# Kernel tuning notes

Measured on AMD Instinct MI355X. Metric: run time of the kernel, lower is better.

## Reference

```python
import jax, jax.numpy as jnp
import numpy as np
from jax import lax

HIDDEN = 16
DN = ('NCHW', 'OIHW', 'NCHW')

def setup_inputs() -> dict:
    key = jax.random.key(0)
    k1, k2, k3 = jax.random.split(key, 3)
    b, t, c, h, w = 8, 12, 5, 256, 256
    x = jax.random.normal(k1, (b, t, c, h, w), dtype=jnp.float32)
    # PyTorch-like init scale for conv weights
    W_cell = jax.random.normal(k2, (4 * HIDDEN, c + HIDDEN, 3, 3), dtype=jnp.float32) * 0.05
    b_cell = jnp.zeros((4 * HIDDEN,), dtype=jnp.float32)
    W_final = jax.random.normal(k3, (1, HIDDEN, 1, 1), dtype=jnp.float32) * 0.1
    b_final = jnp.zeros((1,), dtype=jnp.float32)
    return {"x": x, "W_cell": W_cell, "b_cell": b_cell,
            "W_final": W_final, "b_final": b_final}

def _cell_step(h_c, x_t, W_cell, b_cell):
    h_cur, c_cur = h_c
    combined = jnp.concatenate([x_t, h_cur], axis=1)          # [B, C+H, H, W]
    conv = lax.conv_general_dilated(combined, W_cell, (1, 1), 'SAME',
                                    dimension_numbers=DN)
    conv = conv + b_cell[None, :, None, None]                  # [B, 4H, H, W]
    cc_i, cc_f, cc_o, cc_g = jnp.split(conv, 4, axis=1)
    i = jax.nn.sigmoid(cc_i)
    f = jax.nn.sigmoid(cc_f)
    o = jax.nn.sigmoid(cc_o)
    g = jnp.tanh(cc_g)
    c_next = f * c_cur + i * g
    h_next = o * jnp.tanh(c_next)
    return h_next, c_next

def reference(x, W_cell, b_cell, W_final, b_final):
    b, t, c, hh, ww = x.shape
    h0 = jnp.zeros((b, HIDDEN, hh, ww), dtype=x.dtype)
    c0 = jnp.zeros((b, HIDDEN, hh, ww), dtype=x.dtype)
    xt = jnp.moveaxis(x, 1, 0)  # [T, B, C, H, W] for scan over time

    def step(carry, x_t):
        return _cell_step(carry, x_t, W_cell, b_cell), None

    (h_last, _), _ = lax.scan(step, (h0, c0), xt)
    out = lax.conv_general_dilated(h_last, W_final, (1, 1), 'SAME',
                                   dimension_numbers=DN)
    out = out + b_final[None, :, None, None]
    return out
```

## Files before the change

### kernel.cpp

```cpp
#include <hip/hip_runtime.h>
#include <math.h>

#define HIDDEN 16
#define CIN 5
#define BB 8
#define TT 12
#define HH 256
#define WW 256
#define TX 32
#define TY 8
#define HALO_X 34
#define HALO_Y 10
#define NPX (HALO_X * HALO_Y)
#define STRIDE 40
#define NBLK_PERSIST 1024
#define NTILES 2048

typedef __attribute__((ext_vector_type(8))) short bf16x8;
typedef __attribute__((ext_vector_type(4))) float floatx4;

__device__ __forceinline__ unsigned short f2bf(float f) {
    unsigned int u = __float_as_uint(f);
    u += 0x7fffu + ((u >> 16) & 1u);
    return (unsigned short)(u >> 16);
}
__device__ __forceinline__ float bf2f(unsigned short s) {
    return __uint_as_float(((unsigned int)s) << 16);
}
__device__ __forceinline__ float fast_sigmoid(float x) { return 1.0f / (1.0f + __expf(-x)); }
__device__ __forceinline__ float fast_tanh(float x) {
    float e2 = __expf(-2.0f * fabsf(x));
    float t = (1.0f - e2) / (1.0f + e2);
    return copysignf(t, x);
}

__global__ void prep_w_kernel(const float* __restrict__ Wc,
                              unsigned short* __restrict__ Wfrag) {
    int i = blockIdx.x * 256 + threadIdx.x;
    if (i >= 9 * 4 * 64 * 8) return;
    int j    = i & 7;
    int lane = (i >> 3) & 63;
    int g    = (i >> 9) & 3;
    int tap  = i >> 11;
    int k    = ((lane >> 4) << 3) + j;
    int col  = lane & 15;
    int o    = g * 16 + col;
    float w  = 0.0f;
    if (k < 21) {
        int ci_ref = (k < 16) ? (5 + k) : (k - 16);
        w = Wc[(o * 21 + ci_ref) * 9 + tap];
    }
    Wfrag[i] = f2bf(w);
}

__global__ void prep_x_kernel(const float* __restrict__ x,
                              unsigned short* __restrict__ xp) {
    size_t n = (size_t)blockIdx.x * 256 + threadIdx.x;
    const size_t TOTPX = (size_t)BB * TT * HH * WW;
    if (n >= TOTPX) return;
    size_t bt  = n / (size_t)(HH * WW);
    size_t pix = n - bt * (size_t)(HH * WW);
    const float* src = x + bt * (size_t)CIN * HH * WW + pix;
    unsigned short v[8];
    #pragma unroll
    for (int c = 0; c < CIN; ++c) v[c] = f2bf(src[(size_t)c * HH * WW]);
    v[5] = 0; v[6] = 0; v[7] = 0;
    *(uint4*)&xp[n * 8] = *(const uint4*)v;
}

__global__ void prep_flags_kernel(unsigned int* __restrict__ flags) {
    int i = blockIdx.x * 256 + threadIdx.x;
    if (i < NTILES) flags[i] = 0;
}

__global__ __launch_bounds__(256, 4)
void convlstm_persistent_kernel(const float* __restrict__ x,
                                const unsigned short* __restrict__ xp,
                                unsigned short* __restrict__ ha,
                                unsigned short* __restrict__ hbuf,
                                const unsigned short* __restrict__ Wfrag,
                                const float* __restrict__ bias,
                                const float* __restrict__ Wf,
                                const float* __restrict__ bfin,
                                float* __restrict__ out,
                                unsigned int* __restrict__ flags,
                                int use_xp) {
    __shared__ unsigned short tile[NPX * STRIDE];

    const int tid  = threadIdx.x;
    const int lane = tid & 63;
    const int wave = tid >> 6;
    const int u    = lane & 15;
    const int quad = lane >> 4;
    const int bid  = (int)blockIdx.x;

    int nb_id[2];
    unsigned nb_act = 0;
    {
        int s  = lane + (lane >= 4 ? 1 : 0);
        int dy = s / 3 - 1;
        int dx = s - (s / 3) * 3 - 1;
        #pragma unroll
        for (int tl = 0; tl < 2; ++tl) {
            int n  = bid + tl * NBLK_PERSIST;
            int tx = n & 7;
            int ty = (n >> 3) & 31;
            bool act = (lane < 8) && (tx + dx >= 0) && (tx + dx < 8)
                                  && (ty + dy >= 0) && (ty + dy < 32);
            nb_id[tl] = act ? (n + dy * 8 + dx) : 0;
            if (act) nb_act |= 1u << tl;
        }
    }

    int hof[2][2];
    int xof[2][2];
    int pixv[2][2];
    int bbv[2];
    unsigned inbm = 0;
    #pragma unroll
    for (int tl = 0; tl < 2; ++tl) {
        int n  = bid + tl * NBLK_PERSIST;
        int x0 = (n & 7) * TX;
        int y0 = ((n >> 3) & 31) * TY;
        int bb = n >> 8;
        bbv[tl] = bb;
        #pragma unroll
        for (int it = 0; it < 2; ++it) {
            int i  = tid + it * 256;
            int ly = i / HALO_X;
            int lx = i - ly * HALO_X;
            int gy = y0 + ly - 1;
            int gx = x0 + lx - 1;
            bool inb = (gy >= 0 && gy < HH && gx >= 0 && gx < WW) && (i < NPX);
            int pix = gy * WW + gx;
            pixv[tl][it] = pix;
            hof[tl][it]  = (bb * HH * WW + pix) * HIDDEN;
            xof[tl][it]  = (bb * TT * HH * WW + pix) * 8;
            if (inb) inbm |= 1u << (tl * 2 + it);
        }
    }

    float bg[4];
    #pragma unroll
    for (int g = 0; g < 4; ++g) bg[g] = bias[g * 16 + u];
    const float wfu = Wf[u];
    const float bf0 = bfin[0];

    float cA[2][2][4];
    float cB[2][2][4];
    #pragma unroll
    for (int a = 0; a < 2; ++a)
        #pragma unroll
        for (int m = 0; m < 2; ++m)
            #pragma unroll
            for (int r = 0; r < 4; ++r) { cA[a][m][r] = 0.0f; cB[a][m][r] = 0.0f; }

    #pragma unroll 1
    for (int t = 0; t < TT; ++t) {
        const unsigned short* h_in  = (t & 1) ? ha : hbuf;
        unsigned short*       h_out = (t & 1) ? hbuf : ha;
        const int first = (t == 0);
        const int last  = (t == TT - 1);

        #pragma unroll
        for (int tl = 0; tl < 2; ++tl) {
            const int n  = bid + tl * NBLK_PERSIST;
            const int x0 = (n & 7) * TX;
            const int y0 = ((n >> 3) & 31) * TY;
            const int bb = bbv[tl];

            if (t > 0) {
                if (wave == 0) {
                    const bool act = (nb_act >> tl) & 1;
                    const unsigned need = (unsigned)t;
                    for (;;) {
                        unsigned v = act
                            ? __hip_atomic_load(&flags[nb_id[tl]], __ATOMIC_RELAXED,
                                                __HIP_MEMORY_SCOPE_AGENT)
                            : 0xFFFFFFFFu;
                        if (__all(v >= need)) break;
                        __builtin_amdgcn_s_sleep(2);
                    }
                    if (tid == 0) __threadfence();
                }
                __syncthreads();
            } else if (tl == 1) {
                __syncthreads();
            }

            #pragma unroll
            for (int it = 0; it < 2; ++it) {
                if (it == 1 && tid >= NPX - 256) break;
                unsigned short* row = &tile[(tid + it * 256) * STRIDE];
                const bool inb = (inbm >> (tl * 2 + it)) & 1;
                uint4 z = {0, 0, 0, 0};
                if (inb && !first) {
                    const unsigned short* hp = h_in + hof[tl][it];
                    *(uint4*)&row[0] = *(const uint4*)&hp[0];
                    *(uint4*)&row[8] = *(const uint4*)&hp[8];
                } else {
                    *(uint4*)&row[0] = z;
                    *(uint4*)&row[8] = z;
                }
                if (use_xp) {
                    if (inb)
                        *(uint4*)&row[16] =
                            *(const uint4*)&xp[xof[tl][it] + t * (HH * WW * 8)];
                    else
                        *(uint4*)&row[16] = z;
                } else {
                    #pragma unroll
                    for (int ci = 0; ci < CIN; ++ci) {
                        float v = 0.0f;
                        if (inb) v = x[(((size_t)bb * TT + t) * CIN + ci) * (size_t)(HH * WW)
                                       + pixv[tl][it]];
                        row[16 + ci] = f2bf(v);
                    }
                    row[21] = 0; row[22] = 0; row[23] = 0;
                }
                *(uint4*)&row[24] = z;
            }
            __syncthreads();

            #pragma unroll 1
            for (int half = 0; half < 2; ++half) {
                floatx4 acc[2][4];
                int abase[2];
                #pragma unroll
                for (int mh = 0; mh < 2; ++mh) {
                    int ml = half * 2 + mh;
                    int m  = wave + ml * 4;
                    int my = m >> 1;
                    int mx = (m & 1) << 4;
                    abase[mh] = (my * HALO_X + mx + u) * STRIDE + quad * 8;
                    #pragma unroll
                    for (int g = 0; g < 4; ++g)
                        acc[mh][g] = (floatx4){bg[g], bg[g], bg[g], bg[g]};
                }

                #pragma unroll 3
                for (int tap = 0; tap < 9; ++tap) {
                    int ky = tap / 3;
                    int kx = tap - ky * 3;
                    int toff = (ky * HALO_X + kx) * STRIDE;
                    bf16x8 bfr[4];
                    #pragma unroll
                    for (int g = 0; g < 4; ++g)
                        bfr[g] = *(const bf16x8*)&Wfrag[(size_t)((tap * 4 + g) * 64 + lane) * 8];
                    #pragma unroll
                    for (int mh = 0; mh < 2; ++mh) {
                        bf16x8 af = *(const bf16x8*)&tile[abase[mh] + toff];
                        #pragma unroll
                        for (int g = 0; g < 4; ++g)
                            acc[mh][g] = __builtin_amdgcn_mfma_f32_16x16x32_bf16(
                                af, bfr[g], acc[mh][g], 0, 0, 0);
                    }
                }

                #pragma unroll
                for (int mh = 0; mh < 2; ++mh) {
                    int ml = half * 2 + mh;
                    int m  = wave + ml * 4;
                    int my = m >> 1;
                    int mx = (m & 1) << 4;
                    int py = y0 + my;
                    #pragma unroll
                    for (int r = 0; r < 4; ++r) {
                        int pxx = x0 + mx + quad * 4 + r;
                        float ig = fast_sigmoid(acc[mh][0][r]);
                        float fg = fast_sigmoid(acc[mh][1][r]);
                        float og = fast_sigmoid(acc[mh][2][r]);
                        float gg = fast_tanh(acc[mh][3][r]);
                        float c_old = half ? cB[tl][mh][r] : cA[tl][mh][r];
                        float c_new = fg * c_old + ig * gg;
                        if (half) cB[tl][mh][r] = c_new; else cA[tl][mh][r] = c_new;
                        float hval = og * fast_tanh(c_new);
                        if (last) {
                            float s = wfu * hval;
                            s += __shfl_xor(s, 1);
                            s += __shfl_xor(s, 2);
                            s += __shfl_xor(s, 4);
                            s += __shfl_xor(s, 8);
                            if (u == 0)
                                out[(size_t)bb * HH * WW + (size_t)py * WW + pxx] = s + bf0;
                        } else {
                            size_t idx = ((size_t)bb * HH * WW + (size_t)py * WW + pxx)
                                         * HIDDEN + u;
                            h_out[idx] = f2bf(hval);
                        }
                    }
                }
            }

            if (!last) {
                __syncthreads();
                if (tid == 0) {
                    __threadfence();
                    __hip_atomic_store(&flags[n], (unsigned)(t + 1), __ATOMIC_RELAXED,
                                       __HIP_MEMORY_SCOPE_AGENT);
                }
            }
        }
    }
}

__global__ __launch_bounds__(256, 5)
void convlstm_step_kernel(const float* __restrict__ x, int t,
                          const unsigned short* __restrict__ xp,
                          const unsigned short* __restrict__ h_in,
                          unsigned short* __restrict__ h_out,
                          float* __restrict__ c_state,
                          const unsigned short* __restrict__ Wfrag,
                          const float* __restrict__ bias,
                          int first, int use_xp) {
    __shared__ unsigned short tile[NPX * STRIDE];

    const int tid  = threadIdx.x;
    const int lane = tid & 63;
    const int wave = tid >> 6;
    const int x0 = blockIdx.x * TX;
    const int y0 = blockIdx.y * TY;
    const int bb = blockIdx.z;

    for (int i = tid; i < NPX; i += 256) {
        int ly = i / HALO_X;
        int lx = i - ly * HALO_X;
        int gy = y0 + ly - 1;
        int gx = x0 + lx - 1;
        bool inb = (gy >= 0 && gy < HH && gx >= 0 && gx < WW);
        unsigned short* row = &tile[i * STRIDE];
        uint4 z = {0, 0, 0, 0};
        if (inb && !first) {
            size_t hbase = ((size_t)bb * HH * WW + (size_t)gy * WW + gx) * HIDDEN;
            *(uint4*)&row[0] = *(const uint4*)&h_in[hbase];
            *(uint4*)&row[8] = *(const uint4*)&h_in[hbase + 8];
        } else {
            *(uint4*)&row[0] = z;
            *(uint4*)&row[8] = z;
        }
        if (use_xp) {
            if (inb) {
                size_t xb = (((size_t)bb * TT + t) * (size_t)(HH * WW)
                             + (size_t)gy * WW + gx) * 8;
                *(uint4*)&row[16] = *(const uint4*)&xp[xb];
            } else {
                *(uint4*)&row[16] = z;
            }
        } else {
            #pragma unroll
            for (int ci = 0; ci < CIN; ++ci) {
                float v = 0.0f;
                if (inb) v = x[(((size_t)bb * TT + t) * CIN + ci) * (size_t)(HH * WW)
                               + (size_t)gy * WW + gx];
                row[16 + ci] = f2bf(v);
            }
            row[21] = 0; row[22] = 0; row[23] = 0;
        }
        *(uint4*)&row[24] = z;
    }
    __syncthreads();

    const int u    = lane & 15;
    const int quad = lane >> 4;

    float bg[4];
    #pragma unroll
    for (int g = 0; g < 4; ++g) bg[g] = bias[g * 16 + u];

    #pragma unroll 1
    for (int half = 0; half < 2; ++half) {
        floatx4 acc[2][4];
        int abase[2];
        #pragma unroll
        for (int mh = 0; mh < 2; ++mh) {
            int ml = half * 2 + mh;
            int m  = wave + ml * 4;
            int my = m >> 1;
            int mx = (m & 1) << 4;
            abase[mh] = (my * HALO_X + mx + u) * STRIDE + quad * 8;
            #pragma unroll
            for (int g = 0; g < 4; ++g)
                acc[mh][g] = (floatx4){bg[g], bg[g], bg[g], bg[g]};
        }

        #pragma unroll 3
        for (int tap = 0; tap < 9; ++tap) {
            int ky = tap / 3;
            int kx = tap - ky * 3;
            int toff = (ky * HALO_X + kx) * STRIDE;
            bf16x8 bfr[4];
            #pragma unroll
            for (int g = 0; g < 4; ++g)
                bfr[g] = *(const bf16x8*)&Wfrag[(size_t)((tap * 4 + g) * 64 + lane) * 8];
            #pragma unroll
            for (int mh = 0; mh < 2; ++mh) {
                bf16x8 af = *(const bf16x8*)&tile[abase[mh] + toff];
                #pragma unroll
                for (int g = 0; g < 4; ++g)
                    acc[mh][g] = __builtin_amdgcn_mfma_f32_16x16x32_bf16(
                        af, bfr[g], acc[mh][g], 0, 0, 0);
            }
        }

        #pragma unroll
        for (int mh = 0; mh < 2; ++mh) {
            int ml = half * 2 + mh;
            int m  = wave + ml * 4;
            int my = m >> 1;
            int mx = (m & 1) << 4;
            int py = y0 + my;
            #pragma unroll
            for (int r = 0; r < 4; ++r) {
                int pxx = x0 + mx + quad * 4 + r;
                size_t idx = ((size_t)bb * HH * WW + (size_t)py * WW + pxx) * HIDDEN + u;
                float ig = fast_sigmoid(acc[mh][0][r]);
                float fg = fast_sigmoid(acc[mh][1][r]);
                float og = fast_sigmoid(acc[mh][2][r]);
                float gg = fast_tanh(acc[mh][3][r]);
                float c_old = first ? 0.0f : c_state[idx];
                float c_new = fg * c_old + ig * gg;
                c_state[idx] = c_new;
                h_out[idx] = f2bf(og * fast_tanh(c_new));
            }
        }
    }
}

__global__ void final_conv_kernel(const unsigned short* __restrict__ h,
                                  const float* __restrict__ Wf,
                                  const float* __restrict__ bf_,
                                  float* __restrict__ out) {
    int i = blockIdx.x * 256 + threadIdx.x;
    if (i >= BB * HH * WW) return;
    size_t base = (size_t)i * HIDDEN;
    uint4 v0 = *(const uint4*)&h[base];
    uint4 v1 = *(const uint4*)&h[base + 8];
    const unsigned short* p0 = (const unsigned short*)&v0;
    const unsigned short* p1 = (const unsigned short*)&v1;
    float s = bf_[0];
    #pragma unroll
    for (int k = 0; k < 8; ++k) s += Wf[k] * bf2f(p0[k]);
    #pragma unroll
    for (int k = 0; k < 8; ++k) s += Wf[8 + k] * bf2f(p1[k]);
    out[i] = s;
}

extern "C" void kernel_launch(void* const* d_in, const int* in_sizes, int n_in,
                              void* d_out, int out_size, void* d_ws, size_t ws_size,
                              hipStream_t stream) {
    const float* x  = (const float*)d_in[0];
    const float* Wc = (const float*)d_in[1];
    const float* bc = (const float*)d_in[2];
    const float* Wf = (const float*)d_in[3];
    const float* bf = (const float*)d_in[4];
    float* out = (float*)d_out;

    char* ws = (char*)d_ws;
    const size_t h_bytes = (size_t)BB * HH * WW * HIDDEN * 2;
    const size_t c_bytes = (size_t)BB * HH * WW * HIDDEN * 4;
    const size_t w_bytes = 9 * 4 * 64 * 8 * 2;
    const size_t f_bytes = (size_t)NTILES * 4;
    const size_t x_bytes = (size_t)BB * TT * HH * WW * 8 * 2;

    unsigned short* h_a = (unsigned short*)(ws);
    unsigned short* h_b = (unsigned short*)(ws + h_bytes);
    float* c            = (float*)(ws + 2 * h_bytes);
    unsigned short* Wfr = (unsigned short*)(ws + 2 * h_bytes + c_bytes);
    unsigned int* flags = (unsigned int*)(ws + 2 * h_bytes + c_bytes + w_bytes);
    unsigned short* xp  = (unsigned short*)(ws + 2 * h_bytes + c_bytes + w_bytes + f_bytes);

    const int use_xp =
        (ws_size >= 2 * h_bytes + c_bytes + w_bytes + f_bytes + x_bytes) ? 1 : 0;

    prep_w_kernel<<<(9 * 4 * 64 * 8 + 255) / 256, 256, 0, stream>>>(Wc, Wfr);
    prep_flags_kernel<<<(NTILES + 255) / 256, 256, 0, stream>>>(flags);
    if (use_xp) {
        size_t totpx = (size_t)BB * TT * HH * WW;
        prep_x_kernel<<<(int)((totpx + 255) / 256), 256, 0, stream>>>(x, xp);
    }

    int occ = 0;
    hipOccupancyMaxActiveBlocksPerMultiprocessor(&occ, convlstm_persistent_kernel,
                                                 256, 0);
    bool done = false;
    if (occ >= 4) {
        const unsigned short* xp_arg = use_xp ? xp : (const unsigned short*)0;
        int use_xp_arg = use_xp;
        void* kargs[] = {
            (void*)&x, (void*)&xp_arg, (void*)&h_a, (void*)&h_b,
            (void*)&Wfr, (void*)&bc, (void*)&Wf, (void*)&bf,
            (void*)&out, (void*)&flags, (void*)&use_xp_arg
        };
        if (hipLaunchCooperativeKernel((const void*)convlstm_persistent_kernel,
                                       dim3(NBLK_PERSIST, 1, 1), dim3(256, 1, 1),
                                       kargs, 0, stream) == hipSuccess)
            done = true;
    }

    if (!done) {
        dim3 grid(WW / TX, HH / TY, BB);
        dim3 block(256, 1, 1);
        const unsigned short* h_in = h_a;
        for (int t = 0; t < TT; ++t) {
            unsigned short* h_out = (t & 1) ? h_b : h_a;
            convlstm_step_kernel<<<grid, block, 0, stream>>>(
                x, t, use_xp ? xp : (const unsigned short*)0,
                h_in, h_out, c, Wfr, bc, (t == 0) ? 1 : 0, use_xp);
            h_in = h_out;
        }
        final_conv_kernel<<<(BB * HH * WW + 255) / 256, 256, 0, stream>>>(
            h_in, Wf, bf, out);
    }
}
```

Baseline: 700.4 us.

## Keep hidden state resident in LDS per tile, exchange only halo ring globally

New measurement: 688.7 us. Within noise of the previous version (-1.7%).

```diff
diff --git a/kernel.cpp b/kernel.cpp
--- a/kernel.cpp
+++ b/kernel.cpp
@@ -15,6 +15,9 @@
 #define STRIDE 40
 #define NBLK_PERSIST 1024
 #define NTILES 2048
+#define NRING 84
+#define ROWSH 24
+#define XSTEP (HH * WW * 8)
 
 typedef __attribute__((ext_vector_type(8))) short bf16x8;
 typedef __attribute__((ext_vector_type(4))) float floatx4;
@@ -27,8 +30,21 @@
 __device__ __forceinline__ float bf2f(unsigned short s) {
     return __uint_as_float(((unsigned int)s) << 16);
 }
-__device__ __forceinline__ float fast_sigmoid(float x) { return 1.0f / (1.0f + __expf(-x)); }
+__device__ __forceinline__ float rcpf(float x) {
+    float r;
+    asm("v_rcp_f32 %0, %1" : "=v"(r) : "v"(x));
+    return r;
+}
+__device__ __forceinline__ float fast_sigmoid(float x) {
+    return rcpf(1.0f + __expf(-x));
+}
 __device__ __forceinline__ float fast_tanh(float x) {
+    float e2 = __expf(-2.0f * fabsf(x));
+    float t = (1.0f - e2) * rcpf(1.0f + e2);
+    return copysignf(t, x);
+}
+__device__ __forceinline__ float leg_sigmoid(float x) { return 1.0f / (1.0f + __expf(-x)); }
+__device__ __forceinline__ float leg_tanh(float x) {
     float e2 = __expf(-2.0f * fabsf(x));
     float t = (1.0f - e2) / (1.0f + e2);
     return copysignf(t, x);
@@ -85,7 +101,8 @@
                                 float* __restrict__ out,
                                 unsigned int* __restrict__ flags,
                                 int use_xp) {
-    __shared__ unsigned short tile[NPX * STRIDE];
+    __shared__ unsigned short hx[2 * NPX * ROWSH + 8];
+    const int ZOFF = 2 * NPX * ROWSH;
 
     const int tid  = threadIdx.x;
     const int lane = tid & 63;
@@ -94,6 +111,16 @@
     const int quad = lane >> 4;
     const int bid  = (int)blockIdx.x;
 
+    int ntile[2], x0v[2], y0v[2], bbv[2];
+    #pragma unroll
+    for (int tl = 0; tl < 2; ++tl) {
+        int n = (bid & 7) * 256 + (bid >> 3) + tl * 128;
+        ntile[tl] = n;
+        x0v[tl] = (n & 7) * TX;
+        y0v[tl] = ((n >> 3) & 31) * TY;
+        bbv[tl] = n >> 8;
+    }
+
     int nb_id[2];
     unsigned nb_act = 0;
     {
@@ -102,7 +129,7 @@
         int dx = s - (s / 3) * 3 - 1;
         #pragma unroll
         for (int tl = 0; tl < 2; ++tl) {
-            int n  = bid + tl * NBLK_PERSIST;
+            int n  = ntile[tl];
             int tx = n & 7;
             int ty = (n >> 3) & 31;
             bool act = (lane < 8) && (tx + dx >= 0) && (tx + dx < 8)
@@ -112,39 +139,64 @@
         }
     }
 
-    int hof[2][2];
     int xof[2][2];
     int pixv[2][2];
-    int bbv[2];
     unsigned inbm = 0;
     #pragma unroll
     for (int tl = 0; tl < 2; ++tl) {
-        int n  = bid + tl * NBLK_PERSIST;
-        int x0 = (n & 7) * TX;
-        int y0 = ((n >> 3) & 31) * TY;
-        int bb = n >> 8;
-        bbv[tl] = bb;
         #pragma unroll
         for (int it = 0; it < 2; ++it) {
             int i  = tid + it * 256;
             int ly = i / HALO_X;
             int lx = i - ly * HALO_X;
-            int gy = y0 + ly - 1;
-            int gx = x0 + lx - 1;
+            int gy = y0v[tl] + ly - 1;
+            int gx = x0v[tl] + lx - 1;
             bool inb = (gy >= 0 && gy < HH && gx >= 0 && gx < WW) && (i < NPX);
             int pix = gy * WW + gx;
             pixv[tl][it] = pix;
-            hof[tl][it]  = (bb * HH * WW + pix) * HIDDEN;
-            xof[tl][it]  = (bb * TT * HH * WW + pix) * 8;
+            xof[tl][it]  = (bbv[tl] * TT * HH * WW + pix) * 8;
             if (inb) inbm |= 1u << (tl * 2 + it);
         }
     }
+
+    int rrow = 0;
+    int rgoff[2] = {0, 0};
+    unsigned ringm = 0;
+    if (tid < NRING) {
+        int ly, lx;
+        if (tid < 34)      { ly = 0;                lx = tid; }
+        else if (tid < 68) { ly = HALO_Y - 1;       lx = tid - 34; }
+        else { int k = tid - 68; ly = 1 + (k >> 1); lx = (k & 1) * (HALO_X - 1); }
+        rrow = ly * HALO_X + lx;
+        #pragma unroll
+        for (int tl = 0; tl < 2; ++tl) {
+            int gy = y0v[tl] + ly - 1;
+            int gx = x0v[tl] + lx - 1;
+            bool inb = (gy >= 0 && gy < HH && gx >= 0 && gx < WW);
+            rgoff[tl] = (bbv[tl] * HH * WW + gy * WW + gx) * HIDDEN;
+            if (inb) ringm |= 1u << tl;
+        }
+    }
+
+    uint4 xr0 = {0, 0, 0, 0}, xr1 = {0, 0, 0, 0};
+    if (use_xp) {
+        if (inbm & 1u) xr0 = *(const uint4*)&xp[xof[0][0]];
+        if (tid < NPX - 256 && (inbm & 2u)) xr1 = *(const uint4*)&xp[xof[0][1]];
+    }
+
+    for (int i = tid; i < 2 * NPX; i += 256) {
+        uint4 z = {0, 0, 0, 0};
+        *(uint4*)&hx[i * ROWSH]     = z;
+        *(uint4*)&hx[i * ROWSH + 8] = z;
+    }
+    if (tid == 0) { uint4 z = {0, 0, 0, 0}; *(uint4*)&hx[ZOFF] = z; }
 
     float bg[4];
     #pragma unroll
     for (int g = 0; g < 4; ++g) bg[g] = bias[g * 16 + u];
     const float wfu = Wf[u];
     const float bf0 = bfin[0];
+    const int msel  = (quad < 3) ? ROWSH : 0;
 
     float cA[2][2][4];
     float cB[2][2][4];
@@ -164,10 +216,11 @@
 
         #pragma unroll
         for (int tl = 0; tl < 2; ++tl) {
-            const int n  = bid + tl * NBLK_PERSIST;
-            const int x0 = (n & 7) * TX;
-            const int y0 = ((n >> 3) & 31) * TY;
-            const int bb = bbv[tl];
+            const int n   = ntile[tl];
+            const int x0  = x0v[tl];
+            const int y0  = y0v[tl];
+            const int bb  = bbv[tl];
+            const int TLB = tl * NPX * ROWSH;
 
             if (t > 0) {
                 if (wave == 0) {
@@ -184,55 +237,60 @@
                     if (tid == 0) __threadfence();
                 }
                 __syncthreads();
-            } else if (tl == 1) {
-                __syncthreads();
-            }
-
-            #pragma unroll
-            for (int it = 0; it < 2; ++it) {
-                if (it == 1 && tid >= NPX - 256) break;
-                unsigned short* row = &tile[(tid + it * 256) * STRIDE];
-                const bool inb = (inbm >> (tl * 2 + it)) & 1;
-                uint4 z = {0, 0, 0, 0};
-                if (inb && !first) {
-                    const unsigned short* hp = h_in + hof[tl][it];
-                    *(uint4*)&row[0] = *(const uint4*)&hp[0];
-                    *(uint4*)&row[8] = *(const uint4*)&hp[8];
-                } else {
-                    *(uint4*)&row[0] = z;
-                    *(uint4*)&row[8] = z;
-                }
-                if (use_xp) {
-                    if (inb)
-                        *(uint4*)&row[16] =
-                            *(const uint4*)&xp[xof[tl][it] + t * (HH * WW * 8)];
-                    else
-                        *(uint4*)&row[16] = z;
-                } else {
+            }
+
+            if (use_xp) {
+                *(uint4*)&hx[TLB + tid * ROWSH + 16] = xr0;
+                if (tid < NPX - 256)
+                    *(uint4*)&hx[TLB + (tid + 256) * ROWSH + 16] = xr1;
+            } else {
+                #pragma unroll
+                for (int it = 0; it < 2; ++it) {
+                    if (it == 1 && tid >= NPX - 256) break;
+                    const bool inb = (inbm >> (tl * 2 + it)) & 1;
+                    unsigned short v[8];
                     #pragma unroll
                     for (int ci = 0; ci < CIN; ++ci) {
-                        float v = 0.0f;
-                        if (inb) v = x[(((size_t)bb * TT + t) * CIN + ci) * (size_t)(HH * WW)
+                        float f = 0.0f;
+                        if (inb) f = x[(((size_t)bb * TT + t) * CIN + ci) * (size_t)(HH * WW)
                                        + pixv[tl][it]];
-                        row[16 + ci] = f2bf(v);
+                        v[ci] = f2bf(f);
                     }
-                    row[21] = 0; row[22] = 0; row[23] = 0;
-                }
-                *(uint4*)&row[24] = z;
+                    v[5] = 0; v[6] = 0; v[7] = 0;
+                    *(uint4*)&hx[TLB + (tid + it * 256) * ROWSH + 16] = *(const uint4*)v;
+                }
+            }
+            if (!first && tid < NRING && ((ringm >> tl) & 1)) {
+                const unsigned short* hp = h_in + rgoff[tl];
+                *(uint4*)&hx[TLB + rrow * ROWSH]     = *(const uint4*)&hp[0];
+                *(uint4*)&hx[TLB + rrow * ROWSH + 8] = *(const uint4*)&hp[8];
+            }
+            if (use_xp) {
+                const int ntl = tl ^ 1;
+                const int nt  = t + tl;
+                if (nt < TT) {
+                    uint4 z4 = {0, 0, 0, 0};
+                    xr0 = ((inbm >> (ntl * 2)) & 1)
+                        ? *(const uint4*)&xp[xof[ntl][0] + nt * XSTEP] : z4;
+                    if (tid < NPX - 256)
+                        xr1 = ((inbm >> (ntl * 2 + 1)) & 1)
+                            ? *(const uint4*)&xp[xof[ntl][1] + nt * XSTEP] : z4;
+                }
             }
             __syncthreads();
 
             #pragma unroll 1
             for (int half = 0; half < 2; ++half) {
                 floatx4 acc[2][4];
-                int abase[2];
+                int A[2];
                 #pragma unroll
                 for (int mh = 0; mh < 2; ++mh) {
                     int ml = half * 2 + mh;
                     int m  = wave + ml * 4;
                     int my = m >> 1;
                     int mx = (m & 1) << 4;
-                    abase[mh] = (my * HALO_X + mx + u) * STRIDE + quad * 8;
+                    int bpx = my * HALO_X + mx + u;
+                    A[mh] = (quad < 3) ? (TLB + bpx * ROWSH + quad * 8) : ZOFF;
                     #pragma unroll
                     for (int g = 0; g < 4; ++g)
                         acc[mh][g] = (floatx4){bg[g], bg[g], bg[g], bg[g]};
@@ -242,14 +300,14 @@
                 for (int tap = 0; tap < 9; ++tap) {
                     int ky = tap / 3;
                     int kx = tap - ky * 3;
-                    int toff = (ky * HALO_X + kx) * STRIDE;
+                    int ktap = ky * HALO_X + kx;
                     bf16x8 bfr[4];
                     #pragma unroll
                     for (int g = 0; g < 4; ++g)
                         bfr[g] = *(const bf16x8*)&Wfrag[(size_t)((tap * 4 + g) * 64 + lane) * 8];
                     #pragma unroll
                     for (int mh = 0; mh < 2; ++mh) {
-                        bf16x8 af = *(const bf16x8*)&tile[abase[mh] + toff];
+                        bf16x8 af = *(const bf16x8*)&hx[A[mh] + ktap * msel];
                         #pragma unroll
                         for (int g = 0; g < 4; ++g)
                             acc[mh][g] = __builtin_amdgcn_mfma_f32_16x16x32_bf16(
@@ -264,9 +322,14 @@
                     int my = m >> 1;
                     int mx = (m & 1) << 4;
                     int py = y0 + my;
+                    int col0 = mx + quad * 4;
+                    int erow = (my + 1) * HALO_X + col0 + 1;
+                    int eaddr = TLB + erow * ROWSH + u;
+                    size_t gidx0 = ((size_t)bb * HH * WW + (size_t)py * WW + x0 + col0)
+                                   * HIDDEN + u;
+                    bool topbot = (my == 0) || (my == TY - 1);
                     #pragma unroll
                     for (int r = 0; r < 4; ++r) {
-                        int pxx = x0 + mx + quad * 4 + r;
                         float ig = fast_sigmoid(acc[mh][0][r]);
                         float fg = fast_sigmoid(acc[mh][1][r]);
                         float og = fast_sigmoid(acc[mh][2][r]);
@@ -281,12 +344,16 @@
                             s += __shfl_xor(s, 2);
                             s += __shfl_xor(s, 4);
                             s += __shfl_xor(s, 8);
+                            int col = col0 + r;
                             if (u == 0)
-                                out[(size_t)bb * HH * WW + (size_t)py * WW + pxx] = s + bf0;
+                                out[(size_t)bb * HH * WW + (size_t)py * WW + x0 + col]
+                                    = s + bf0;
                         } else {
-                            size_t idx = ((size_t)bb * HH * WW + (size_t)py * WW + pxx)
-                                         * HIDDEN + u;
-                            h_out[idx] = f2bf(hval);
+                            unsigned short hs = f2bf(hval);
+                            hx[eaddr + r * ROWSH] = hs;
+                            int col = col0 + r;
+                            if (topbot || col == 0 || col == TX - 1)
+                                h_out[gidx0 + (size_t)r * HIDDEN] = hs;
                         }
                     }
                 }
@@ -413,14 +480,14 @@
             for (int r = 0; r < 4; ++r) {
                 int pxx = x0 + mx + quad * 4 + r;
                 size_t idx = ((size_t)bb * HH * WW + (size_t)py * WW + pxx) * HIDDEN + u;
-                float ig = fast_sigmoid(acc[mh][0][r]);
-                float fg = fast_sigmoid(acc[mh][1][r]);
-                float og = fast_sigmoid(acc[mh][2][r]);
-                float gg = fast_tanh(acc[mh][3][r]);
+                float ig = leg_sigmoid(acc[mh][0][r]);
+                float fg = leg_sigmoid(acc[mh][1][r]);
+                float og = leg_sigmoid(acc[mh][2][r]);
+                float gg = leg_tanh(acc[mh][3][r]);
                 float c_old = first ? 0.0f : c_state[idx];
                 float c_new = fg * c_old + ig * gg;
                 c_state[idx] = c_new;
-                h_out[idx] = f2bf(og * fast_tanh(c_new));
+                h_out[idx] = f2bf(og * leg_tanh(c_new));
             }
         }
     }
```

## Shrink persistent tiles to 32x4, stage weights in LDS, drop zero K-quad

Applied to the files above, without the earlier changes.

After: 715.5 us. 1.02x slower.

```diff
diff --git a/kernel.cpp b/kernel.cpp
--- a/kernel.cpp
+++ b/kernel.cpp
@@ -13,8 +13,21 @@
 #define HALO_Y 10
 #define NPX (HALO_X * HALO_Y)
 #define STRIDE 40
+#define PTX 32
+#define PTY 4
+#define PHX 34
+#define PHY 6
+#define PNPX (PHX * PHY)
+#define ROWSH 24
+#define NTILES 4096
 #define NBLK_PERSIST 1024
-#define NTILES 2048
+#define XSTEP (HH * WW * 8)
+#define WSH (9 * 4 * 48 * 8)
+#define WSH_PAD (WSH + 8)
+#define TILE_SH (PNPX * ROWSH)
+#define WOFF TILE_SH
+#define ZOFF (TILE_SH + WSH)
+#define SMSH (TILE_SH + WSH_PAD)
 
 typedef __attribute__((ext_vector_type(8))) short bf16x8;
 typedef __attribute__((ext_vector_type(4))) float floatx4;
@@ -27,8 +40,21 @@
 __device__ __forceinline__ float bf2f(unsigned short s) {
     return __uint_as_float(((unsigned int)s) << 16);
 }
-__device__ __forceinline__ float fast_sigmoid(float x) { return 1.0f / (1.0f + __expf(-x)); }
+__device__ __forceinline__ float rcpf(float x) {
+    float r;
+    asm("v_rcp_f32 %0, %1" : "=v"(r) : "v"(x));
+    return r;
+}
+__device__ __forceinline__ float fast_sigmoid(float x) {
+    return rcpf(1.0f + __expf(-x));
+}
 __device__ __forceinline__ float fast_tanh(float x) {
+    float e2 = __expf(-2.0f * fabsf(x));
+    float t = (1.0f - e2) * rcpf(1.0f + e2);
+    return copysignf(t, x);
+}
+__device__ __forceinline__ float leg_sigmoid(float x) { return 1.0f / (1.0f + __expf(-x)); }
+__device__ __forceinline__ float leg_tanh(float x) {
     float e2 = __expf(-2.0f * fabsf(x));
     float t = (1.0f - e2) / (1.0f + e2);
     return copysignf(t, x);
@@ -37,11 +63,14 @@
 __global__ void prep_w_kernel(const float* __restrict__ Wc,
                               unsigned short* __restrict__ Wfrag) {
     int i = blockIdx.x * 256 + threadIdx.x;
-    if (i >= 9 * 4 * 64 * 8) return;
+    if (i >= WSH_PAD) return;
+    if (i >= WSH) { Wfrag[i] = 0; return; }
     int j    = i & 7;
-    int lane = (i >> 3) & 63;
-    int g    = (i >> 9) & 3;
-    int tap  = i >> 11;
+    int t8   = i >> 3;
+    int lane = t8 % 48;
+    int t48  = t8 / 48;
+    int g    = t48 & 3;
+    int tap  = t48 >> 2;
     int k    = ((lane >> 4) << 3) + j;
     int col  = lane & 15;
     int o    = g * 16 + col;
@@ -85,7 +114,7 @@
                                 float* __restrict__ out,
                                 unsigned int* __restrict__ flags,
                                 int use_xp) {
-    __shared__ unsigned short tile[NPX * STRIDE];
+    __shared__ unsigned short sm[SMSH];
 
     const int tid  = threadIdx.x;
     const int lane = tid & 63;
@@ -94,51 +123,30 @@
     const int quad = lane >> 4;
     const int bid  = (int)blockIdx.x;
 
-    int nb_id[2];
-    unsigned nb_act = 0;
+    const int bb = bid >> 7;
+    const int ty = (bid >> 1) & 63;
+    const int y0 = ty * PTY;
+    const int n0 = bid * 4;
+
+    for (int i = tid; i < WSH_PAD / 8; i += 256)
+        *(uint4*)&sm[WOFF + i * 8] = *(const uint4*)&Wfrag[i * 8];
+
+    const int wbl   = (lane < 48) ? (WOFF + lane * 8) : ZOFF;
+    const int wstep = (lane < 48) ? 384 : 0;
+
+    int nb_dy = 0, nb_dx = 0;
     {
         int s  = lane + (lane >= 4 ? 1 : 0);
-        int dy = s / 3 - 1;
-        int dx = s - (s / 3) * 3 - 1;
-        #pragma unroll
-        for (int tl = 0; tl < 2; ++tl) {
-            int n  = bid + tl * NBLK_PERSIST;
-            int tx = n & 7;
-            int ty = (n >> 3) & 31;
-            bool act = (lane < 8) && (tx + dx >= 0) && (tx + dx < 8)
-                                  && (ty + dy >= 0) && (ty + dy < 32);
-            nb_id[tl] = act ? (n + dy * 8 + dx) : 0;
-            if (act) nb_act |= 1u << tl;
-        }
-    }
-
-    int hof[2][2];
-    int xof[2][2];
-    int pixv[2][2];
-    int bbv[2];
-    unsigned inbm = 0;
-    #pragma unroll
-    for (int tl = 0; tl < 2; ++tl) {
-        int n  = bid + tl * NBLK_PERSIST;
-        int x0 = (n & 7) * TX;
-        int y0 = ((n >> 3) & 31) * TY;
-        int bb = n >> 8;
-        bbv[tl] = bb;
-        #pragma unroll
-        for (int it = 0; it < 2; ++it) {
-            int i  = tid + it * 256;
-            int ly = i / HALO_X;
-            int lx = i - ly * HALO_X;
-            int gy = y0 + ly - 1;
-            int gx = x0 + lx - 1;
-            bool inb = (gy >= 0 && gy < HH && gx >= 0 && gx < WW) && (i < NPX);
-            int pix = gy * WW + gx;
-            pixv[tl][it] = pix;
-            hof[tl][it]  = (bb * HH * WW + pix) * HIDDEN;
-            xof[tl][it]  = (bb * TT * HH * WW + pix) * 8;
-            if (inb) inbm |= 1u << (tl * 2 + it);
-        }
-    }
+        nb_dy = s / 3 - 1;
+        nb_dx = s - (s / 3) * 3 - 1;
+    }
+
+    const int sly = tid / PHX;
+    const int slx = tid - sly * PHX;
+    const int gy  = y0 + sly - 1;
+    const bool yok = (gy >= 0) && (gy < HH);
+    const int hbase_y = (bb * HH * WW + gy * WW) * HIDDEN;
+    const int xbase_y = (bb * TT * HH * WW + gy * WW) * 8;
 
     float bg[4];
     #pragma unroll
@@ -146,14 +154,21 @@
     const float wfu = Wf[u];
     const float bf0 = bfin[0];
 
-    float cA[2][2][4];
-    float cB[2][2][4];
-    #pragma unroll
-    for (int a = 0; a < 2; ++a)
+    int A[2];
+    #pragma unroll
+    for (int mh = 0; mh < 2; ++mh)
+        A[mh] = (quad < 3) ? ((wave * PHX + mh * 16 + u) * ROWSH + quad * 8)
+                           : ZOFF;
+    const int msel = (quad < 3) ? ROWSH : 0;
+
+    float cV0[2][4], cV1[2][4], cV2[2][4], cV3[2][4];
+    #pragma unroll
+    for (int m = 0; m < 2; ++m)
         #pragma unroll
-        for (int m = 0; m < 2; ++m)
-            #pragma unroll
-            for (int r = 0; r < 4; ++r) { cA[a][m][r] = 0.0f; cB[a][m][r] = 0.0f; }
+        for (int r = 0; r < 4; ++r) {
+            cV0[m][r] = 0.0f; cV1[m][r] = 0.0f;
+            cV2[m][r] = 0.0f; cV3[m][r] = 0.0f;
+        }
 
     #pragma unroll 1
     for (int t = 0; t < TT; ++t) {
@@ -162,40 +177,38 @@
         const int first = (t == 0);
         const int last  = (t == TT - 1);
 
-        #pragma unroll
-        for (int tl = 0; tl < 2; ++tl) {
-            const int n  = bid + tl * NBLK_PERSIST;
-            const int x0 = (n & 7) * TX;
-            const int y0 = ((n >> 3) & 31) * TY;
-            const int bb = bbv[tl];
+        #pragma unroll 1
+        for (int v = 0; v < 4; ++v) {
+            const int n  = n0 + v;
+            const int tx = n & 7;
+            const int x0 = tx * PTX;
 
             if (t > 0) {
                 if (wave == 0) {
-                    const bool act = (nb_act >> tl) & 1;
+                    bool act = (lane < 8) && (tx + nb_dx >= 0) && (tx + nb_dx < 8)
+                                          && (ty + nb_dy >= 0) && (ty + nb_dy < 64);
+                    int nb = n + nb_dy * 8 + nb_dx;
                     const unsigned need = (unsigned)t;
                     for (;;) {
-                        unsigned v = act
-                            ? __hip_atomic_load(&flags[nb_id[tl]], __ATOMIC_RELAXED,
+                        unsigned fv = act
+                            ? __hip_atomic_load(&flags[nb], __ATOMIC_RELAXED,
                                                 __HIP_MEMORY_SCOPE_AGENT)
                             : 0xFFFFFFFFu;
-                        if (__all(v >= need)) break;
+                        if (__all(fv >= need)) break;
                         __builtin_amdgcn_s_sleep(2);
                     }
                     if (tid == 0) __threadfence();
                 }
                 __syncthreads();
-            } else if (tl == 1) {
-                __syncthreads();
-            }
-
-            #pragma unroll
-            for (int it = 0; it < 2; ++it) {
-                if (it == 1 && tid >= NPX - 256) break;
-                unsigned short* row = &tile[(tid + it * 256) * STRIDE];
-                const bool inb = (inbm >> (tl * 2 + it)) & 1;
+            }
+
+            if (tid < PNPX) {
+                unsigned short* row = &sm[tid * ROWSH];
                 uint4 z = {0, 0, 0, 0};
+                int gx = x0 + slx - 1;
+                bool inb = yok && ((unsigned)gx < (unsigned)WW);
                 if (inb && !first) {
-                    const unsigned short* hp = h_in + hof[tl][it];
+                    const unsigned short* hp = h_in + hbase_y + gx * HIDDEN;
                     *(uint4*)&row[0] = *(const uint4*)&hp[0];
                     *(uint4*)&row[8] = *(const uint4*)&hp[8];
                 } else {
@@ -205,100 +218,88 @@
                 if (use_xp) {
                     if (inb)
                         *(uint4*)&row[16] =
-                            *(const uint4*)&xp[xof[tl][it] + t * (HH * WW * 8)];
+                            *(const uint4*)&xp[xbase_y + t * XSTEP + gx * 8];
                     else
                         *(uint4*)&row[16] = z;
                 } else {
+                    unsigned short vv[8];
                     #pragma unroll
                     for (int ci = 0; ci < CIN; ++ci) {
-                        float v = 0.0f;
-                        if (inb) v = x[(((size_t)bb * TT + t) * CIN + ci) * (size_t)(HH * WW)
-                                       + pixv[tl][it]];
-                        row[16 + ci] = f2bf(v);
+                        float f = 0.0f;
+                        if (inb) f = x[(((size_t)bb * TT + t) * CIN + ci)
+                                       * (size_t)(HH * WW) + gy * WW + gx];
+                        vv[ci] = f2bf(f);
                     }
-                    row[21] = 0; row[22] = 0; row[23] = 0;
+                    vv[5] = 0; vv[6] = 0; vv[7] = 0;
+                    *(uint4*)&row[16] = *(const uint4*)vv;
                 }
-                *(uint4*)&row[24] = z;
             }
             __syncthreads();
 
-            #pragma unroll 1
-            for (int half = 0; half < 2; ++half) {
-                floatx4 acc[2][4];
-                int abase[2];
+            floatx4 acc[2][4];
+            #pragma unroll
+            for (int mh = 0; mh < 2; ++mh)
+                #pragma unroll
+                for (int g = 0; g < 4; ++g)
+                    acc[mh][g] = (floatx4){bg[g], bg[g], bg[g], bg[g]};
+
+            #pragma unroll 3
+            for (int tap = 0; tap < 9; ++tap) {
+                int ky = tap / 3;
+                int kx = tap - ky * 3;
+                int ktap = ky * PHX + kx;
+                bf16x8 bfr[4];
+                #pragma unroll
+                for (int g = 0; g < 4; ++g)
+                    bfr[g] = *(const bf16x8*)&sm[wbl + (tap * 4 + g) * wstep];
                 #pragma unroll
                 for (int mh = 0; mh < 2; ++mh) {
-                    int ml = half * 2 + mh;
-                    int m  = wave + ml * 4;
-                    int my = m >> 1;
-                    int mx = (m & 1) << 4;
-                    abase[mh] = (my * HALO_X + mx + u) * STRIDE + quad * 8;
+                    bf16x8 af = *(const bf16x8*)&sm[A[mh] + ktap * msel];
                     #pragma unroll
                     for (int g = 0; g < 4; ++g)
-                        acc[mh][g] = (floatx4){bg[g], bg[g], bg[g], bg[g]};
+                        acc[mh][g] = __builtin_amdgcn_mfma_f32_16x16x32_bf16(
+                            af, bfr[g], acc[mh][g], 0, 0, 0);
                 }
-
-                #pragma unroll 3
-                for (int tap = 0; tap < 9; ++tap) {
-                    int ky = tap / 3;
-                    int kx = tap - ky * 3;
-                    int toff = (ky * HALO_X + kx) * STRIDE;
-                    bf16x8 bfr[4];
-                    #pragma unroll
-                    for (int g = 0; g < 4; ++g)
-                        bfr[g] = *(const bf16x8*)&Wfrag[(size_t)((tap * 4 + g) * 64 + lane) * 8];
-                    #pragma unroll
-                    for (int mh = 0; mh < 2; ++mh) {
-                        bf16x8 af = *(const bf16x8*)&tile[abase[mh] + toff];
-                        #pragma unroll
-                        for (int g = 0; g < 4; ++g)
-                            acc[mh][g] = __builtin_amdgcn_mfma_f32_16x16x32_bf16(
-                                af, bfr[g], acc[mh][g], 0, 0, 0);
+            }
+
+            #pragma unroll
+            for (int mh = 0; mh < 2; ++mh) {
+                int py = y0 + wave;
+                int col0 = mh * 16 + quad * 4;
+                size_t gidx0 = ((size_t)bb * HH * WW + (size_t)py * WW + x0 + col0)
+                               * HIDDEN + u;
+                #pragma unroll
+                for (int r = 0; r < 4; ++r) {
+                    float ig = fast_sigmoid(acc[mh][0][r]);
+                    float fg = fast_sigmoid(acc[mh][1][r]);
+                    float og = fast_sigmoid(acc[mh][2][r]);
+                    float gg = fast_tanh(acc[mh][3][r]);
+                    float c_old = (v & 2) ? ((v & 1) ? cV3[mh][r] : cV2[mh][r])
+                                          : ((v & 1) ? cV1[mh][r] : cV0[mh][r]);
+                    float c_new = fg * c_old + ig * gg;
+                    if (v & 2) { if (v & 1) cV3[mh][r] = c_new; else cV2[mh][r] = c_new; }
+                    else       { if (v & 1) cV1[mh][r] = c_new; else cV0[mh][r] = c_new; }
+                    float hval = og * fast_tanh(c_new);
+                    if (last) {
+                        float s = wfu * hval;
+                        s += __shfl_xor(s, 1);
+                        s += __shfl_xor(s, 2);
+                        s += __shfl_xor(s, 4);
+                        s += __shfl_xor(s, 8);
+                        if (u == 0)
+                            out[(size_t)bb * HH * WW + (size_t)py * WW + x0 + col0 + r]
+                                = s + bf0;
+                    } else {
+                        h_out[gidx0 + (size_t)r * HIDDEN] = f2bf(hval);
                     }
                 }
-
-                #pragma unroll
-                for (int mh = 0; mh < 2; ++mh) {
-                    int ml = half * 2 + mh;
-                    int m  = wave + ml * 4;
-                    int my = m >> 1;
-                    int mx = (m & 1) << 4;
-                    int py = y0 + my;
-                    #pragma unroll
-                    for (int r = 0; r < 4; ++r) {
-                        int pxx = x0 + mx + quad * 4 + r;
-                        float ig = fast_sigmoid(acc[mh][0][r]);
-                        float fg = fast_sigmoid(acc[mh][1][r]);
-                        float og = fast_sigmoid(acc[mh][2][r]);
-                        float gg = fast_tanh(acc[mh][3][r]);
-                        float c_old = half ? cB[tl][mh][r] : cA[tl][mh][r];
-                        float c_new = fg * c_old + ig * gg;
-                        if (half) cB[tl][mh][r] = c_new; else cA[tl][mh][r] = c_new;
-                        float hval = og * fast_tanh(c_new);
-                        if (last) {
-                            float s = wfu * hval;
-                            s += __shfl_xor(s, 1);
-                            s += __shfl_xor(s, 2);
-                            s += __shfl_xor(s, 4);
-                            s += __shfl_xor(s, 8);
-                            if (u == 0)
-                                out[(size_t)bb * HH * WW + (size_t)py * WW + pxx] = s + bf0;
-                        } else {
-                            size_t idx = ((size_t)bb * HH * WW + (size_t)py * WW + pxx)
-                                         * HIDDEN + u;
-                            h_out[idx] = f2bf(hval);
-                        }
-                    }
-                }
-            }
-
-            if (!last) {
-                __syncthreads();
-                if (tid == 0) {
-                    __threadfence();
-                    __hip_atomic_store(&flags[n], (unsigned)(t + 1), __ATOMIC_RELAXED,
-                                       __HIP_MEMORY_SCOPE_AGENT);
-                }
+            }
+
+            __syncthreads();
+            if (!last && tid == 0) {
+                __threadfence();
+                __hip_atomic_store(&flags[n], (unsigned)(t + 1), __ATOMIC_RELAXED,
+                                   __HIP_MEMORY_SCOPE_AGENT);
             }
         }
     }
@@ -363,6 +364,9 @@
     const int u    = lane & 15;
     const int quad = lane >> 4;
 
+    const unsigned short* wptr = (lane < 48) ? (Wfrag + lane * 8) : (Wfrag + WSH);
+    const int wstep2 = (lane < 48) ? 384 : 0;
+
     float bg[4];
     #pragma unroll
     for (int g = 0; g < 4; ++g) bg[g] = bias[g * 16 + u];
@@ -391,7 +395,7 @@
             bf16x8 bfr[4];
             #pragma unroll
             for (int g = 0; g < 4; ++g)
-                bfr[g] = *(const bf16x8*)&Wfrag[(size_t)((tap * 4 + g) * 64 + lane) * 8];
+                bfr[g] = *(const bf16x8*)&wptr[(tap * 4 + g) * wstep2];
             #pragma unroll
             for (int mh = 0; mh < 2; ++mh) {
                 bf16x8 af = *(const bf16x8*)&tile[abase[mh] + toff];
@@ -413,14 +417,14 @@
             for (int r = 0; r < 4; ++r) {
                 int pxx = x0 + mx + quad * 4 + r;
                 size_t idx = ((size_t)bb * HH * WW + (size_t)py * WW + pxx) * HIDDEN + u;
-                float ig = fast_sigmoid(acc[mh][0][r]);
-                float fg = fast_sigmoid(acc[mh][1][r]);
-                float og = fast_sigmoid(acc[mh][2][r]);
-                float gg = fast_tanh(acc[mh][3][r]);
+                float ig = leg_sigmoid(acc[mh][0][r]);
+                float fg = leg_sigmoid(acc[mh][1][r]);
+                float og = leg_sigmoid(acc[mh][2][r]);
+                float gg = leg_tanh(acc[mh][3][r]);
                 float c_old = first ? 0.0f : c_state[idx];
                 float c_new = fg * c_old + ig * gg;
                 c_state[idx] = c_new;
-                h_out[idx] = f2bf(og * fast_tanh(c_new));
+                h_out[idx] = f2bf(og * leg_tanh(c_new));
             }
         }
     }
@@ -458,7 +462,7 @@
     char* ws = (char*)d_ws;
     const size_t h_bytes = (size_t)BB * HH * WW * HIDDEN * 2;
     const size_t c_bytes = (size_t)BB * HH * WW * HIDDEN * 4;
-    const size_t w_bytes = 9 * 4 * 64 * 8 * 2;
+    const size_t w_bytes = (size_t)WSH_PAD * 2;
     const size_t f_bytes = (size_t)NTILES * 4;
     const size_t x_bytes = (size_t)BB * TT * HH * WW * 8 * 2;
 
@@ -472,7 +476,7 @@
     const int use_xp =
         (ws_size >= 2 * h_bytes + c_bytes + w_bytes + f_bytes + x_bytes) ? 1 : 0;
 
-    prep_w_kernel<<<(9 * 4 * 64 * 8 + 255) / 256, 256, 0, stream>>>(Wc, Wfr);
+    prep_w_kernel<<<(WSH_PAD + 255) / 256, 256, 0, stream>>>(Wc, Wfr);
     prep_flags_kernel<<<(NTILES + 255) / 256, 256, 0, stream>>>(flags);
     if (use_xp) {
         size_t totpx = (size_t)BB * TT * HH * WW;
```
